# Kernel tuning notes

Hardware: AMD Instinct MI355X
Metric: run time of the kernel (lower is better)

## Reference

```python
import jax, jax.numpy as jnp
import numpy as np

B, S, H, C, V, NC = 128, 512, 128, 16, 32000, 8
EPS = 1e-4

def _summarize(centers, spreads, masses):
    precision = 1.0 / (spreads + EPS)
    scores = masses + jnp.log(precision + EPS)
    alpha = jax.nn.softmax(scores, axis=-1)                      # [B,C]
    core = jnp.einsum('bc,bch->bh', alpha, centers)              # [B,H]
    uncertainty = jnp.sum(alpha * spreads, -1, keepdims=True)
    sq_dist = jnp.mean((centers - core[:, None, :]) ** 2, -1)    # [B,C]
    diversity = jnp.sum(alpha * sq_dist, -1, keepdims=True)
    energy = jax.nn.logsumexp(masses, axis=-1, keepdims=True)
    entropy = -jnp.sum(alpha * jnp.log(jnp.clip(alpha, 1e-8)), -1, keepdims=True)
    return core, uncertainty, diversity, energy, entropy, alpha

def _interaction(centers, spreads, masses):
    sq = jnp.sum(centers ** 2, -1)                               # [B,C]
    d2 = jnp.maximum(sq[:, :, None] + sq[:, None, :] - 2.0 * jnp.einsum('bih,bjh->bij', centers, centers), 0.0)
    scale = spreads[:, :, None] + spreads[:, None, :] + EPS
    compat = -d2 / scale + masses[:, None, :]
    mixing = jax.nn.softmax(compat, axis=-1)                     # [B,C,C]
    mixed_centers = jnp.einsum('bij,bjh->bih', mixing, centers)
    mixed_spreads = jnp.sum(mixing * spreads[:, None, :], -1)
    mixed_masses = jnp.sum(mixing * masses[:, None, :], -1)
    return mixed_centers, mixed_spreads, mixed_masses

def _forward(tokens, emb, ln_g, ln_b, ctrl_w1, ctrl_b1, ctrl_w2, ctrl_b2,
             gate_w, gate_b, assign_w, assign_b, nov_w, nov_b, relax_w, relax_b,
             cc_w, cc_b, cs_w, cs_b, md_w, md_b, att_w, att_b,
             cls_w1, cls_b1, cls_w2, cls_b2):
    emb = emb.at[0].set(0.0)  # padding_idx row zero
    mask = (tokens != 0).astype(jnp.float32)                     # [B,S]
    e = emb[tokens]                                              # [B,S,H]
    mu = e.mean(-1, keepdims=True)
    var = e.var(-1, keepdims=True)
    te = (e - mu) / jnp.sqrt(var + 1e-5) * ln_g + ln_b           # LayerNorm

    def step(state, x):
        centers, spreads, masses = state
        token_t, valid = x                                       # [B,H], [B,1]
        core, u, d, en, ent, _ = _summarize(centers, spreads, masses)
        ci = jnp.concatenate([token_t, core, u, d, en, ent], -1) # [B,2H+4]
        ctrl = jnp.tanh(jnp.tanh(ci @ ctrl_w1 + ctrl_b1) @ ctrl_w2 + ctrl_b2)
        gate = jax.nn.sigmoid(ctrl @ gate_w + gate_b) * valid
        assign = jax.nn.softmax(ctrl @ assign_w + assign_b, axis=-1)
        novelty = jax.nn.sigmoid(ctrl @ nov_w + nov_b) * valid
        relax = jax.nn.sigmoid(ctrl @ relax_w + relax_b) * valid
        cand_c = (ctrl @ cc_w + cc_b).reshape(token_t.shape[0], C, H)
        cand_s = jax.nn.softplus(ctrl @ cs_w + cs_b) + EPS
        mdelta = jnp.tanh(ctrl @ md_w + md_b)
        ss = gate * assign                                       # [B,C]
        centers = centers + ss[..., None] * (cand_c - centers)
        spreads = spreads + ss * (cand_s - spreads)
        masses = masses + ss * mdelta
        # attractor + reconfiguration always fire (sparse_reconfiguration=False)
        attractor = (ctrl @ att_w + att_b)[:, None, :]
        centers = centers + 0.1 * novelty[..., None] * (attractor - centers)
        mc, ms, mm = _interaction(centers, spreads, masses)
        centers = (1.0 - relax[..., None]) * centers + relax[..., None] * mc
        spreads = (1.0 - relax) * spreads + relax * ms
        masses = (1.0 - relax) * masses + relax * mm
        precision = 1.0 / (spreads + EPS)
        ca = jax.nn.softmax(masses + jnp.log(precision + EPS), axis=-1)
        spreads = spreads * (1.0 - 0.05 * ca * valid) + EPS
        return (centers, spreads, masses), None

    init = (jnp.zeros((B, C, H)), jnp.ones((B, C)), jnp.zeros((B, C)))
    xs = (jnp.swapaxes(te, 0, 1), mask.T[:, :, None])            # [S,B,H], [S,B,1]
    (centers, spreads, masses), _ = jax.lax.scan(jax.checkpoint(step), init, xs)

    core, u, d, en, ent, alpha = _summarize(centers, spreads, masses)
    idx = jnp.argmax(alpha, axis=-1)                             # [B]
    strongest = jnp.take_along_axis(centers, idx[:, None, None], axis=1)[:, 0, :]
    feats = jnp.concatenate([core, strongest, u, d, en, ent], -1)
    h = jax.nn.gelu(feats @ cls_w1 + cls_b1, approximate=False)
    return h @ cls_w2 + cls_b2                                   # [B,NC]


def setup_inputs() -> dict:
    key = jax.random.key(0)
    ks = jax.random.split(key, 32)
    def rn(i, shape, s=0.05):
        return jax.random.normal(ks[i], shape, jnp.float32) * s
    CI = 2 * H + 4
    return {
        'tokens': jax.random.randint(ks[0], (B, S), 0, V),
        'emb': rn(1, (V, H), 1.0).at[0].set(0.0),
        'ln_g': jnp.ones((H,), jnp.float32),
        'ln_b': jnp.zeros((H,), jnp.float32),
        'ctrl_w1': rn(2, (CI, H)), 'ctrl_b1': rn(3, (H,)),
        'ctrl_w2': rn(4, (H, H)), 'ctrl_b2': rn(5, (H,)),
        'gate_w': rn(6, (H, C)), 'gate_b': rn(7, (C,)),
        'assign_w': rn(8, (H, C)), 'assign_b': rn(9, (C,)),
        'nov_w': rn(10, (H, 1)), 'nov_b': rn(11, (1,)),
        'relax_w': rn(12, (H, 1)), 'relax_b': rn(13, (1,)),
        'cc_w': rn(14, (H, C * H)), 'cc_b': rn(15, (C * H,)),
        'cs_w': rn(16, (H, C)), 'cs_b': rn(17, (C,)),
        'md_w': rn(18, (H, C)), 'md_b': rn(19, (C,)),
        'att_w': rn(20, (H, H)), 'att_b': rn(21, (H,)),
        'cls_w1': rn(22, (CI, H)), 'cls_b1': rn(23, (H,)),
        'cls_w2': rn(24, (H, NC)), 'cls_b2': rn(25, (NC,)),
    }


def reference(tokens, emb, ln_g, ln_b, ctrl_w1, ctrl_b1, ctrl_w2, ctrl_b2,
              gate_w, gate_b, assign_w, assign_b, nov_w, nov_b, relax_w, relax_b,
              cc_w, cc_b, cs_w, cs_b, md_w, md_b, att_w, att_b,
              cls_w1, cls_b1, cls_w2, cls_b2):
    return _forward(tokens, emb, ln_g, ln_b, ctrl_w1, ctrl_b1, ctrl_w2, ctrl_b2,
                    gate_w, gate_b, assign_w, assign_b, nov_w, nov_b, relax_w, relax_b,
                    cc_w, cc_b, cs_w, cs_b, md_w, md_b, att_w, att_b,
                    cls_w1, cls_b1, cls_w2, cls_b2)
```

## Files before the change

kernel.cpp:

```cpp
#include <hip/hip_runtime.h>
#include <hip/hip_fp16.h>
#include <math.h>

#define NB   128
#define SEQ  512
#define HD   128
#define NCL  16
#define NOUT 8
#define CIP  272
#define FEPS 1e-4f
#define HP   132

#define FMA4(cc, W4) { a0 = fmaf((cc),(W4).x,a0); a1 = fmaf((cc),(W4).y,a1); a2 = fmaf((cc),(W4).z,a2); a3 = fmaf((cc),(W4).w,a3); }

__device__ __forceinline__ float red16(float v){
    v += __shfl_xor(v, 1, 16); v += __shfl_xor(v, 2, 16);
    v += __shfl_xor(v, 4, 16); v += __shfl_xor(v, 8, 16);
    return v;
}
__device__ __forceinline__ float max16(float v){
    v = fmaxf(v, __shfl_xor(v, 1, 16)); v = fmaxf(v, __shfl_xor(v, 2, 16));
    v = fmaxf(v, __shfl_xor(v, 4, 16)); v = fmaxf(v, __shfl_xor(v, 8, 16));
    return v;
}
__device__ __forceinline__ float red64(float v){
    v += __shfl_xor(v, 1, 64); v += __shfl_xor(v, 2, 64); v += __shfl_xor(v, 4, 64);
    v += __shfl_xor(v, 8, 64); v += __shfl_xor(v,16, 64); v += __shfl_xor(v,32, 64);
    return v;
}
__device__ __forceinline__ float sigm(float x){ return 1.f/(1.f + expf(-x)); }
__device__ __forceinline__ float softplusf(float x){ return log1pf(expf(-fabsf(x))) + fmaxf(x, 0.f); }

__global__ __launch_bounds__(256)
void convert_ccw(const float* __restrict__ src, __half* __restrict__ dst){
    int i = blockIdx.x*256 + threadIdx.x;
    int k2 = i >> 9;
    int jg = i & 511;
    float4 va = ((const float4*)(src + (size_t)(2*k2)*2048))[jg];
    float4 vb = ((const float4*)(src + (size_t)(2*k2+1)*2048))[jg];
    __half2 h0 = __floats2half2_rn(va.x, vb.x);
    __half2 h1 = __floats2half2_rn(va.y, vb.y);
    __half2 h2 = __floats2half2_rn(va.z, vb.z);
    __half2 h3 = __floats2half2_rn(va.w, vb.w);
    __half2* o = (__half2*)dst + (size_t)k2*2048 + jg*4;
    o[0]=h0; o[1]=h1; o[2]=h2; o[3]=h3;
}

template<int USE16>
__global__ __launch_bounds__(512)
void cfrm_kernel(const int*  __restrict__ tokens,
                 const float* __restrict__ emb,
                 const float* __restrict__ ln_g, const float* __restrict__ ln_b,
                 const float* __restrict__ w1,   const float* __restrict__ b1,
                 const float* __restrict__ w2,   const float* __restrict__ b2,
                 const float* __restrict__ gate_w, const float* __restrict__ gate_b,
                 const float* __restrict__ assign_w, const float* __restrict__ assign_b,
                 const float* __restrict__ nov_w, const float* __restrict__ nov_b,
                 const float* __restrict__ relax_w, const float* __restrict__ relax_b,
                 const float* __restrict__ cc_w, const float* __restrict__ cc_b,
                 const __half* __restrict__ ccw_h,
                 const float* __restrict__ cs_w, const float* __restrict__ cs_b,
                 const float* __restrict__ md_w, const float* __restrict__ md_b,
                 const float* __restrict__ att_w, const float* __restrict__ att_b,
                 const float* __restrict__ cw1,  const float* __restrict__ cb1,
                 const float* __restrict__ cw2,  const float* __restrict__ cb2,
                 float* __restrict__ out)
{
    const int bidx = blockIdx.x;
    const int tid  = threadIdx.x;
    const int lane = tid & 63;
    const int wv   = tid >> 6;

    __shared__ __align__(16) float s_w1[260][HD];
    __shared__ __align__(16) float s_centers[NCL][HP];
    __shared__ __align__(16) float s_ci[CIP];
    __shared__ __align__(16) float s_ctrl1[HD];
    __shared__ __align__(16) float s_ctrl[HD];
    __shared__ __align__(16) float s_red16[16][HD];
    __shared__ __align__(16) float s_hred[4][NCL];
    __shared__ __align__(16) float s_att[HD];
    __shared__ __align__(16) float s_gram[NCL][NCL+1];
    __shared__ __align__(16) float s_mix[NCL][NCL+1];
    __shared__ float s_alpha[NCL], s_spreads[NCL], s_masses[NCL];
    __shared__ float s_ss[NCL], s_cands[NCL], s_mdl[NCL];
    __shared__ float s_ms[NCL], s_mm[NCL];
    __shared__ float s_scal[2];
    __shared__ int   s_ibest;
    __shared__ int   s_tok[SEQ];

    {
        const float4* w1f4 = (const float4*)w1;
        float4* s_w1f4 = (float4*)s_w1;
        for (int idx = tid; idx < 260*32; idx += 512) s_w1f4[idx] = w1f4[idx];
    }

    for (int i = tid; i < NCL*HP; i += 512) ((float*)s_centers)[i] = 0.f;
    if (tid >= 260 && tid < CIP) s_ci[tid] = 0.f;
    if (tid < NCL){ s_spreads[tid] = 1.f; s_masses[tid] = 0.f; }
    s_tok[tid] = tokens[bidx*SEQ + tid];

    float rb1 = 0.f, rb2 = 0.f, ratt = 0.f, rw257 = 0.f;
    if (tid < HD){ rb1 = b1[tid]; rb2 = b2[tid]; ratt = att_b[tid]; rw257 = w1[257*HD + tid]; }
    float rg0=0.f, rg1=0.f, rlb0=0.f, rlb1=0.f;
    if (wv == 0){ rg0 = ln_g[lane]; rg1 = ln_g[64+lane]; rlb0 = ln_b[lane]; rlb1 = ln_b[64+lane]; }
    float rgb=0.f, rab=0.f, rcb=0.f, rmb=0.f;
    if (wv == 2 && lane < NCL){ rgb = gate_b[lane]; rab = assign_b[lane]; rcb = cs_b[lane]; rmb = md_b[lane]; }
    float rnw0=0.f, rnw1=0.f, rrw0=0.f, rrw1=0.f, rnb=0.f, rrb=0.f;
    if (wv == 3){ rnw0 = nov_w[lane]; rnw1 = nov_w[64+lane]; rrw0 = relax_w[lane]; rrw1 = relax_w[64+lane];
                  rnb = nov_b[0]; rrb = relax_b[0]; }

    const int j0 = tid*4, ci_c = j0 >> 7, ci_h = j0 & 127;
    const float4 ccb4 = *(const float4*)(cc_b + j0);
    const float* wp = cc_w + j0;
    const __half2* pk = (const __half2*)ccw_h + tid*4;

    const int jj   = (tid & 31)*4;
    const int part = tid >> 5;
    const int k0w1 = part*17;
    const int k0w2 = part*8;

    const int parta = (tid >> 5) & 7;
    const int k0a   = parta*16;
    const float* hwp = gate_w; int c4i = 0, k0h = 0;
    if (wv >= 4){
        int head = wv - 4;
        hwp = (head==0) ? gate_w : (head==1) ? assign_w : (head==2) ? cs_w : md_w;
        c4i = lane & 3; k0h = (lane >> 2)*8;
    }

    __syncthreads();

    float e0c = 0.f, e1c = 0.f;
    if (wv == 0){
        int t0 = s_tok[0];
        e0c = emb[(size_t)t0*HD + lane];
        e1c = emb[(size_t)t0*HD + 64 + lane];
    }

    for (int s = 0; s < SEQ; ++s){
        const int tok = s_tok[s];
        const float valid = (tok != 0) ? 1.f : 0.f;

        float e0n = 0.f, e1n = 0.f;
        if (wv == 0 && s + 1 < SEQ){
            int tn = s_tok[s+1];
            e0n = emb[(size_t)tn*HD + lane];
            e1n = emb[(size_t)tn*HD + 64 + lane];
        }

        if (wv == 0){
            float sm = red64(e0c + e1c);
            float sq = red64(e0c*e0c + e1c*e1c);
            float mu  = sm * (1.f/128.f);
            float var = sq * (1.f/128.f) - mu*mu;
            float inv = 1.f / sqrtf(var + 1e-5f);
            s_ci[lane]      = (e0c - mu)*inv*rg0 + rlb0;
            s_ci[64 + lane] = (e1c - mu)*inv*rg1 + rlb1;
        }
        if (wv == 1 && lane < NCL){
            float sp = s_spreads[lane], ma = s_masses[lane];
            float prec = 1.f/(sp + FEPS);
            float sc = ma + logf(prec + FEPS);
            float mx = max16(sc);
            float ex = expf(sc - mx);
            float smn = red16(ex);
            float al = ex / smn;
            s_alpha[lane] = al;
            float u = red16(al * sp);
            float mmx = max16(ma);
            float es = red16(expf(ma - mmx));
            float en = mmx + logf(es);
            float ent = -red16(al * logf(fmaxf(al, 1e-8f)));
            if (lane == 0){ s_ci[256] = u; s_ci[258] = en; s_ci[259] = ent; }
        }
        __syncthreads();

        if (tid < HD){
            float acc = 0.f;
            #pragma unroll
            for (int c = 0; c < NCL; ++c) acc += s_alpha[c] * s_centers[c][tid];
            s_ci[128 + tid] = acc;
        }
        __syncthreads();

        if (wv == 0){
            int c = lane >> 2, p = lane & 3;
            float acc = 0.f;
            #pragma unroll 8
            for (int hh = p*32; hh < p*32 + 32; ++hh){
                float d = s_centers[c][hh] - s_ci[128 + hh];
                acc += d*d;
            }
            acc += __shfl_xor(acc, 1, 4); acc += __shfl_xor(acc, 2, 4);
            float v = ((lane & 3) == 0) ? s_alpha[c]*acc*(1.f/128.f) : 0.f;
            v = red64(v);
            if (lane == 0) s_ci[257] = v;
        }
        {
            float a0=0.f,a1=0.f,a2=0.f,a3=0.f;
            #pragma unroll
            for (int u = 0; u < 17; ++u){
                int k = k0w1 + u;
                int kc = (k < 260) ? k : 0;
                float cv = (k == 257) ? 0.f : s_ci[k];
                float4 w4 = *(const float4*)&s_w1[kc][jj];
                FMA4(cv, w4)
            }
            *(float4*)&s_red16[part][jj] = make_float4(a0,a1,a2,a3);
        }
        __syncthreads();

        if (tid < HD){
            float acc = rb1 + rw257 * s_ci[257];
            #pragma unroll
            for (int p = 0; p < 16; ++p) acc += s_red16[p][tid];
            s_ctrl1[tid] = tanhf(acc);
        }
        __syncthreads();

        {
            float a0=0.f,a1=0.f,a2=0.f,a3=0.f;
            #pragma unroll
            for (int u = 0; u < 8; ++u){
                int k = k0w2 + u;
                float4 w4 = *(const float4*)(w2 + k*HD + jj);
                float cl = s_ctrl1[k];
                FMA4(cl, w4)
            }
            *(float4*)&s_red16[part][jj] = make_float4(a0,a1,a2,a3);
        }
        __syncthreads();

        if (tid < HD){
            float acc = rb2;
            #pragma unroll
            for (int p = 0; p < 16; ++p) acc += s_red16[p][tid];
            s_ctrl[tid] = tanhf(acc);
        }
        __syncthreads();

        float a0=0.f, a1=0.f, a2=0.f, a3=0.f;
        if constexpr (USE16){
            #pragma unroll 8
            for (int k2 = 0; k2 < 64; ++k2){
                float c0 = s_ctrl[2*k2], c1 = s_ctrl[2*k2+1];
                float4 raw = *(const float4*)(pk + (k2 << 11));
                const __half2* h2p = (const __half2*)&raw;
                float2 f0 = __half22float2(h2p[0]);
                float2 f1 = __half22float2(h2p[1]);
                float2 f2 = __half22float2(h2p[2]);
                float2 f3 = __half22float2(h2p[3]);
                a0 = fmaf(c0,f0.x,fmaf(c1,f0.y,a0));
                a1 = fmaf(c0,f1.x,fmaf(c1,f1.y,a1));
                a2 = fmaf(c0,f2.x,fmaf(c1,f2.y,a2));
                a3 = fmaf(c0,f3.x,fmaf(c1,f3.y,a3));
            }
        } else {
            #pragma unroll 16
            for (int k = 0; k < HD; ++k){
                float cl = s_ctrl[k];
                float4 w4 = *(const float4*)(wp + ((size_t)k << 11));
                FMA4(cl, w4)
            }
        }
        if (tid < 256){
            float t0=0.f,t1=0.f,t2=0.f,t3=0.f;
            #pragma unroll 8
            for (int u = 0; u < 16; ++u){
                int k = k0a + u;
                float4 w4 = *(const float4*)(att_w + k*HD + jj);
                float cl = s_ctrl[k];
                t0 = fmaf(cl, w4.x, t0); t1 = fmaf(cl, w4.y, t1);
                t2 = fmaf(cl, w4.z, t2); t3 = fmaf(cl, w4.w, t3);
            }
            *(float4*)&s_red16[parta][jj] = make_float4(t0,t1,t2,t3);
        } else {
            float4 acc = make_float4(0.f,0.f,0.f,0.f);
            #pragma unroll
            for (int u = 0; u < 8; ++u){
                int k = k0h + u;
                float4 hT = *(const float4*)(hwp + k*NCL + c4i*4);
                float cl = s_ctrl[k];
                acc.x = fmaf(cl, hT.x, acc.x);
                acc.y = fmaf(cl, hT.y, acc.y);
                acc.z = fmaf(cl, hT.z, acc.z);
                acc.w = fmaf(cl, hT.w, acc.w);
            }
            #pragma unroll
            for (int m = 4; m <= 32; m <<= 1){
                acc.x += __shfl_xor(acc.x, m, 64);
                acc.y += __shfl_xor(acc.y, m, 64);
                acc.z += __shfl_xor(acc.z, m, 64);
                acc.w += __shfl_xor(acc.w, m, 64);
            }
            if (lane < 4) *(float4*)&s_hred[wv-4][lane*4] = acc;
        }
        __syncthreads();

        if (tid < HD){
            float acc = ratt;
            #pragma unroll
            for (int p = 0; p < 8; ++p) acc += s_red16[p][tid];
            s_att[tid] = acc;
        } else if (wv == 2 && lane < NCL){
            int c = lane;
            float g    = sigm(s_hred[0][c] + rgb) * valid;
            float araw = s_hred[1][c] + rab;
            float mx = max16(araw);
            float ex = expf(araw - mx);
            float smn = red16(ex);
            s_ss[c]    = g * (ex / smn);
            s_cands[c] = softplusf(s_hred[2][c] + rcb) + FEPS;
            s_mdl[c]   = tanhf(s_hred[3][c] + rmb);
        } else if (wv == 3){
            float c0 = s_ctrl[lane], c1v = s_ctrl[64 + lane];
            float np = red64(c0*rnw0 + c1v*rnw1);
            float rp = red64(c0*rrw0 + c1v*rrw1);
            if (lane == 0){
                s_scal[0] = sigm(np + rnb) * valid;
                s_scal[1] = sigm(rp + rrb) * valid;
            }
        }
        __syncthreads();

        {
            float ssc = s_ss[ci_c];
            float nv  = s_scal[0];
            float4 av = *(const float4*)&s_att[ci_h];
            float4* cp = (float4*)&s_centers[ci_c][ci_h];
            float4 ov = *cp;
            float x0 = ov.x + ssc*((a0 + ccb4.x) - ov.x); x0 = fmaf(0.1f*nv, av.x - x0, x0);
            float x1 = ov.y + ssc*((a1 + ccb4.y) - ov.y); x1 = fmaf(0.1f*nv, av.y - x1, x1);
            float x2 = ov.z + ssc*((a2 + ccb4.z) - ov.z); x2 = fmaf(0.1f*nv, av.z - x2, x2);
            float x3 = ov.w + ssc*((a3 + ccb4.w) - ov.w); x3 = fmaf(0.1f*nv, av.w - x3, x3);
            *cp = make_float4(x0, x1, x2, x3);
        }
        if (tid < NCL){
            float ssc = s_ss[tid];
            s_spreads[tid] += ssc * (s_cands[tid] - s_spreads[tid]);
            s_masses[tid]  += ssc * s_mdl[tid];
        }
        __syncthreads();

        if (tid < 256){
            int gi = tid >> 4, gj = tid & 15;
            const float4* ri = (const float4*)&s_centers[gi][0];
            const float4* rj = (const float4*)&s_centers[gj][0];
            float acc = 0.f;
            #pragma unroll 8
            for (int h4 = 0; h4 < 32; ++h4){
                float4 a = ri[h4], b = rj[h4];
                acc = fmaf(a.x,b.x,fmaf(a.y,b.y,fmaf(a.z,b.z,fmaf(a.w,b.w,acc))));
            }
            s_gram[gi][gj] = acc;
        }
        __syncthreads();

        if (tid < 256){
            int i = tid >> 4, jx = tid & 15;
            float g  = s_gram[i][jx];
            float d2 = fmaxf(s_gram[i][i] + s_gram[jx][jx] - 2.f*g, 0.f);
            float scale = s_spreads[i] + s_spreads[jx] + FEPS;
            float cmp = -d2/scale + s_masses[jx];
            float mx = max16(cmp);
            float ex = expf(cmp - mx);
            float smn = red16(ex);
            float mix = ex / smn;
            s_mix[i][jx] = mix;
            float msp = red16(mix * s_spreads[jx]);
            float mma = red16(mix * s_masses[jx]);
            if (jx == 0){ s_ms[i] = msp; s_mm[i] = mma; }
        }
        __syncthreads();

        {
            int i = tid & 15, hh = (tid >> 4)*4;
            float t0=0.f,t1=0.f,t2=0.f,t3=0.f;
            #pragma unroll
            for (int jc = 0; jc < NCL; ++jc){
                float m = s_mix[i][jc];
                float4 cv = *(const float4*)&s_centers[jc][hh];
                t0 = fmaf(m, cv.x, t0); t1 = fmaf(m, cv.y, t1);
                t2 = fmaf(m, cv.z, t2); t3 = fmaf(m, cv.w, t3);
            }
            float rx = s_scal[1];
            float4* cp2 = (float4*)&s_centers[i][hh];
            float4 ov = *cp2;
            ov.x = (1.f - rx)*ov.x + rx*t0;
            ov.y = (1.f - rx)*ov.y + rx*t1;
            ov.z = (1.f - rx)*ov.z + rx*t2;
            ov.w = (1.f - rx)*ov.w + rx*t3;
            *cp2 = ov;
        }
        if (tid < NCL){
            float rx = s_scal[1];
            float sp = (1.f - rx)*s_spreads[tid] + rx*s_ms[tid];
            float ma = (1.f - rx)*s_masses[tid]  + rx*s_mm[tid];
            float prec = 1.f/(sp + FEPS);
            float sc = ma + logf(prec + FEPS);
            float mx = max16(sc);
            float ex = expf(sc - mx);
            float smn = red16(ex);
            float ca = ex / smn;
            s_spreads[tid] = sp*(1.f - 0.05f*ca*valid) + FEPS;
            s_masses[tid]  = ma;
        }
        e0c = e0n; e1c = e1n;
        __syncthreads();
    }

    if (tid < NCL){
        float sp = s_spreads[tid], ma = s_masses[tid];
        float prec = 1.f/(sp + FEPS);
        float sc = ma + logf(prec + FEPS);
        float mx = max16(sc);
        float ex = expf(sc - mx);
        float smn = red16(ex);
        float al = ex / smn;
        s_alpha[tid] = al;
        float u = red16(al * sp);
        float mmx = max16(ma);
        float es = red16(expf(ma - mmx));
        float en = mmx + logf(es);
        float ent = -red16(al * logf(fmaxf(al, 1e-8f)));
        if (tid == 0){ s_ci[256] = u; s_ci[258] = en; s_ci[259] = ent; }
    }
    __syncthreads();
    if (tid < HD){
        float acc = 0.f;
        #pragma unroll
        for (int c = 0; c < NCL; ++c) acc += s_alpha[c] * s_centers[c][tid];
        s_ci[tid] = acc;
    }
    __syncthreads();
    if (wv == 0){
        int c = lane >> 2, p = lane & 3;
        float acc = 0.f;
        #pragma unroll 8
        for (int hh = p*32; hh < p*32 + 32; ++hh){
            float d = s_centers[c][hh] - s_ci[hh];
            acc += d*d;
        }
        acc += __shfl_xor(acc, 1, 4); acc += __shfl_xor(acc, 2, 4);
        float v = ((lane & 3) == 0) ? s_alpha[c]*acc*(1.f/128.f) : 0.f;
        v = red64(v);
        if (lane == 0) s_ci[257] = v;
    }
    if (wv == 1 && lane == 0){
        int best = 0; float bv = s_alpha[0];
        for (int c = 1; c < NCL; ++c){ if (s_alpha[c] > bv){ bv = s_alpha[c]; best = c; } }
        s_ibest = best;
    }
    __syncthreads();
    if (tid < HD) s_ci[128 + tid] = s_centers[s_ibest][tid];
    __syncthreads();
    {
        int j = tid & 127, p4 = tid >> 7;
        int k0 = p4*65;
        float acc = 0.f;
        for (int k = k0; k < k0 + 65; ++k) acc += s_ci[k] * cw1[k*HD + j];
        s_red16[p4][j] = acc;
    }
    __syncthreads();
    if (tid < HD){
        float x = cb1[tid] + s_red16[0][tid] + s_red16[1][tid] + s_red16[2][tid] + s_red16[3][tid];
        s_ctrl1[tid] = 0.5f*x*(1.f + erff(x*0.70710678118654752f));
    }
    __syncthreads();
    if (tid < 64){
        int n = tid >> 3, p = tid & 7;
        float acc = 0.f;
        #pragma unroll
        for (int kk = 0; kk < 16; ++kk){ int jx = p*16 + kk; acc += s_ctrl1[jx] * cw2[jx*NOUT + n]; }
        acc += __shfl_xor(acc, 1, 8); acc += __shfl_xor(acc, 2, 8); acc += __shfl_xor(acc, 4, 8);
        if (p == 0) out[bidx*NOUT + n] = acc + cb2[n];
    }
}

extern "C" void kernel_launch(void* const* d_in, const int* in_sizes, int n_in,
                              void* d_out, int out_size, void* d_ws, size_t ws_size,
                              hipStream_t stream) {
    const int*   tokens   = (const int*)  d_in[0];
    const float* emb      = (const float*)d_in[1];
    const float* ln_g     = (const float*)d_in[2];
    const float* ln_b     = (const float*)d_in[3];
    const float* ctrl_w1  = (const float*)d_in[4];
    const float* ctrl_b1  = (const float*)d_in[5];
    const float* ctrl_w2  = (const float*)d_in[6];
    const float* ctrl_b2  = (const float*)d_in[7];
    const float* gate_w   = (const float*)d_in[8];
    const float* gate_b   = (const float*)d_in[9];
    const float* assign_w = (const float*)d_in[10];
    const float* assign_b = (const float*)d_in[11];
    const float* nov_w    = (const float*)d_in[12];
    const float* nov_b    = (const float*)d_in[13];
    const float* relax_w  = (const float*)d_in[14];
    const float* relax_b  = (const float*)d_in[15];
    const float* cc_w     = (const float*)d_in[16];
    const float* cc_b     = (const float*)d_in[17];
    const float* cs_w     = (const float*)d_in[18];
    const float* cs_b     = (const float*)d_in[19];
    const float* md_w     = (const float*)d_in[20];
    const float* md_b     = (const float*)d_in[21];
    const float* att_w    = (const float*)d_in[22];
    const float* att_b    = (const float*)d_in[23];
    const float* cls_w1   = (const float*)d_in[24];
    const float* cls_b1   = (const float*)d_in[25];
    const float* cls_w2   = (const float*)d_in[26];
    const float* cls_b2   = (const float*)d_in[27];
    float* out = (float*)d_out;

    const size_t need = (size_t)2048 * 128 * sizeof(__half);
    if (ws_size >= need){
        __half* ccw_h = (__half*)d_ws;
        hipLaunchKernelGGL(convert_ccw, dim3(128), dim3(256), 0, stream, cc_w, ccw_h);
        hipLaunchKernelGGL((cfrm_kernel<1>), dim3(NB), dim3(512), 0, stream,
                           tokens, emb, ln_g, ln_b,
                           ctrl_w1, ctrl_b1, ctrl_w2, ctrl_b2,
                           gate_w, gate_b, assign_w, assign_b,
                           nov_w, nov_b, relax_w, relax_b,
                           cc_w, cc_b, ccw_h, cs_w, cs_b, md_w, md_b,
                           att_w, att_b, cls_w1, cls_b1, cls_w2, cls_b2,
                           out);
    } else {
        hipLaunchKernelGGL((cfrm_kernel<0>), dim3(NB), dim3(512), 0, stream,
                           tokens, emb, ln_g, ln_b,
                           ctrl_w1, ctrl_b1, ctrl_w2, ctrl_b2,
                           gate_w, gate_b, assign_w, assign_b,
                           nov_w, nov_b, relax_w, relax_b,
                           cc_w, cc_b, (const __half*)nullptr, cs_w, cs_b, md_w, md_b,
                           att_w, att_b, cls_w1, cls_b1, cls_w2, cls_b2,
                           out);
    }
}
```

Measured before the change: 8.667 ms.

## Move summary softmax to end of step and cut per-step barriers and reductions

Computes the next step's cluster alpha, uncertainty, energy and entropy at the end of each recurrent step, right after spreads and masses are updated, instead of at the start of the following step. This removes one barrier per step and lets the core computation run alongside the LayerNorm. The controller matvec partial sums are first halved with a cross-lane shuffle, so the shared reduction buffer shrinks from 16 rows to 8. The next-token embedding prefetch is moved later in the loop, which shortens register live ranges but hides less latency.

```diff
diff --git a/kernel.cpp b/kernel.cpp
--- a/kernel.cpp
+++ b/kernel.cpp
@@ -76,7 +76,7 @@
     __shared__ __align__(16) float s_ci[CIP];
     __shared__ __align__(16) float s_ctrl1[HD];
     __shared__ __align__(16) float s_ctrl[HD];
-    __shared__ __align__(16) float s_red16[16][HD];
+    __shared__ __align__(16) float s_red16[8][HD];
     __shared__ __align__(16) float s_hred[4][NCL];
     __shared__ __align__(16) float s_att[HD];
     __shared__ __align__(16) float s_gram[NCL][NCL+1];
@@ -96,7 +96,6 @@
 
     for (int i = tid; i < NCL*HP; i += 512) ((float*)s_centers)[i] = 0.f;
     if (tid >= 260 && tid < CIP) s_ci[tid] = 0.f;
-    if (tid < NCL){ s_spreads[tid] = 1.f; s_masses[tid] = 0.f; }
     s_tok[tid] = tokens[bidx*SEQ + tid];
 
     float rb1 = 0.f, rb2 = 0.f, ratt = 0.f, rw257 = 0.f;
@@ -128,6 +127,22 @@
         c4i = lane & 3; k0h = (lane >> 2)*8;
     }
 
+    if (tid < NCL){
+        s_spreads[tid] = 1.f; s_masses[tid] = 0.f;
+        float sp = 1.f, ma = 0.f;
+        float prec = 1.f/(sp + FEPS);
+        float sc = ma + logf(prec + FEPS);
+        float mx = max16(sc);
+        float ex = expf(sc - mx);
+        float smn = red16(ex);
+        float al = ex / smn;
+        s_alpha[tid] = al;
+        float u = red16(al * sp);
+        float mmx = max16(ma);
+        float es = red16(expf(ma - mmx));
+        float ent = -red16(al * logf(fmaxf(al, 1e-8f)));
+        if (tid == 0){ s_ci[256] = u; s_ci[258] = mmx + logf(es); s_ci[259] = ent; }
+    }
     __syncthreads();
 
     float e0c = 0.f, e1c = 0.f;
@@ -140,13 +155,7 @@
     for (int s = 0; s < SEQ; ++s){
         const int tok = s_tok[s];
         const float valid = (tok != 0) ? 1.f : 0.f;
-
         float e0n = 0.f, e1n = 0.f;
-        if (wv == 0 && s + 1 < SEQ){
-            int tn = s_tok[s+1];
-            e0n = emb[(size_t)tn*HD + lane];
-            e1n = emb[(size_t)tn*HD + 64 + lane];
-        }
 
         if (wv == 0){
             float sm = red64(e0c + e1c);
@@ -156,30 +165,12 @@
             float inv = 1.f / sqrtf(var + 1e-5f);
             s_ci[lane]      = (e0c - mu)*inv*rg0 + rlb0;
             s_ci[64 + lane] = (e1c - mu)*inv*rg1 + rlb1;
-        }
-        if (wv == 1 && lane < NCL){
-            float sp = s_spreads[lane], ma = s_masses[lane];
-            float prec = 1.f/(sp + FEPS);
-            float sc = ma + logf(prec + FEPS);
-            float mx = max16(sc);
-            float ex = expf(sc - mx);
-            float smn = red16(ex);
-            float al = ex / smn;
-            s_alpha[lane] = al;
-            float u = red16(al * sp);
-            float mmx = max16(ma);
-            float es = red16(expf(ma - mmx));
-            float en = mmx + logf(es);
-            float ent = -red16(al * logf(fmaxf(al, 1e-8f)));
-            if (lane == 0){ s_ci[256] = u; s_ci[258] = en; s_ci[259] = ent; }
-        }
-        __syncthreads();
-
-        if (tid < HD){
+        } else if (wv == 1 || wv == 2){
+            int t = tid - 64;
             float acc = 0.f;
             #pragma unroll
-            for (int c = 0; c < NCL; ++c) acc += s_alpha[c] * s_centers[c][tid];
-            s_ci[128 + tid] = acc;
+            for (int c = 0; c < NCL; ++c) acc += s_alpha[c] * s_centers[c][t];
+            s_ci[128 + t] = acc;
         }
         __syncthreads();
 
@@ -206,14 +197,16 @@
                 float4 w4 = *(const float4*)&s_w1[kc][jj];
                 FMA4(cv, w4)
             }
-            *(float4*)&s_red16[part][jj] = make_float4(a0,a1,a2,a3);
+            a0 += __shfl_xor(a0,32); a1 += __shfl_xor(a1,32);
+            a2 += __shfl_xor(a2,32); a3 += __shfl_xor(a3,32);
+            if (lane < 32) *(float4*)&s_red16[wv][jj] = make_float4(a0,a1,a2,a3);
         }
         __syncthreads();
 
         if (tid < HD){
             float acc = rb1 + rw257 * s_ci[257];
             #pragma unroll
-            for (int p = 0; p < 16; ++p) acc += s_red16[p][tid];
+            for (int p = 0; p < 8; ++p) acc += s_red16[p][tid];
             s_ctrl1[tid] = tanhf(acc);
         }
         __syncthreads();
@@ -227,18 +220,25 @@
                 float cl = s_ctrl1[k];
                 FMA4(cl, w4)
             }
-            *(float4*)&s_red16[part][jj] = make_float4(a0,a1,a2,a3);
+            a0 += __shfl_xor(a0,32); a1 += __shfl_xor(a1,32);
+            a2 += __shfl_xor(a2,32); a3 += __shfl_xor(a3,32);
+            if (lane < 32) *(float4*)&s_red16[wv][jj] = make_float4(a0,a1,a2,a3);
         }
         __syncthreads();
 
         if (tid < HD){
             float acc = rb2;
             #pragma unroll
-            for (int p = 0; p < 16; ++p) acc += s_red16[p][tid];
+            for (int p = 0; p < 8; ++p) acc += s_red16[p][tid];
             s_ctrl[tid] = tanhf(acc);
         }
         __syncthreads();
 
+        if (wv == 0 && s + 1 < SEQ){
+            int tn = s_tok[s+1];
+            e0n = emb[(size_t)tn*HD + lane];
+            e1n = emb[(size_t)tn*HD + 64 + lane];
+        }
         float a0=0.f, a1=0.f, a2=0.f, a3=0.f;
         if constexpr (USE16){
             #pragma unroll 8
@@ -402,30 +402,26 @@
             float ex = expf(sc - mx);
             float smn = red16(ex);
             float ca = ex / smn;
-            s_spreads[tid] = sp*(1.f - 0.05f*ca*valid) + FEPS;
+            sp = sp*(1.f - 0.05f*ca*valid) + FEPS;
+            s_spreads[tid] = sp;
             s_masses[tid]  = ma;
+            float prec2 = 1.f/(sp + FEPS);
+            float sc2 = ma + logf(prec2 + FEPS);
+            float mx2 = max16(sc2);
+            float ex2 = expf(sc2 - mx2);
+            float sm2 = red16(ex2);
+            float al = ex2 / sm2;
+            s_alpha[tid] = al;
+            float u = red16(al * sp);
+            float mmx = max16(ma);
+            float es = red16(expf(ma - mmx));
+            float ent = -red16(al * logf(fmaxf(al, 1e-8f)));
+            if (tid == 0){ s_ci[256] = u; s_ci[258] = mmx + logf(es); s_ci[259] = ent; }
         }
         e0c = e0n; e1c = e1n;
         __syncthreads();
     }
 
-    if (tid < NCL){
-        float sp = s_spreads[tid], ma = s_masses[tid];
-        float prec = 1.f/(sp + FEPS);
-        float sc = ma + logf(prec + FEPS);
-        float mx = max16(sc);
-        float ex = expf(sc - mx);
-        float smn = red16(ex);
-        float al = ex / smn;
-        s_alpha[tid] = al;
-        float u = red16(al * sp);
-        float mmx = max16(ma);
-        float es = red16(expf(ma - mmx));
-        float en = mmx + logf(es);
-        float ent = -red16(al * logf(fmaxf(al, 1e-8f)));
-        if (tid == 0){ s_ci[256] = u; s_ci[258] = en; s_ci[259] = ent; }
-    }
-    __syncthreads();
     if (tid < HD){
         float acc = 0.f;
         #pragma unroll
```

New measurement: 8.715 ms. Within noise of the previous version (+0.5%).
